# Optimization experiments

Measured on AMD Instinct MI355X. Metric: run time of the kernel, lower is better.

The kernel has to match this reference:

```python
import jax, jax.numpy as jnp
import numpy as np
import math

N_HEADS = 12
D_MODEL = 768
D_HEAD = 64
IGNORE = -100000.0
INIT_STD = 0.02


def setup_inputs() -> dict:
    key = jax.random.key(0)
    ks = jax.random.split(key, 8)
    b, s = 4, 1024
    return {
        "normalized_resid_pre": jax.random.normal(ks[0], (b, 1, s, D_MODEL), jnp.float32),
        "alt_normalized_resid_pre": jax.random.normal(ks[1], (b, s, D_MODEL), jnp.float32),
        "W_Q": jax.random.normal(ks[2], (N_HEADS, D_MODEL, D_HEAD), jnp.float32) * INIT_STD,
        "b_Q": jnp.zeros((N_HEADS, D_HEAD), jnp.float32),
        "W_K": jax.random.normal(ks[3], (N_HEADS, D_MODEL, D_HEAD), jnp.float32) * INIT_STD,
        "b_K": jnp.zeros((N_HEADS, D_HEAD), jnp.float32),
        "W_V": jax.random.normal(ks[4], (N_HEADS, D_MODEL, D_HEAD), jnp.float32) * INIT_STD,
        "b_V": jnp.zeros((N_HEADS, D_HEAD), jnp.float32),
        "W_O": jax.random.normal(ks[5], (N_HEADS, D_HEAD, D_MODEL), jnp.float32) * INIT_STD,
        "b_O": jnp.zeros((D_MODEL,), jnp.float32),
    }


def _apply_attention(x, W_Q, b_Q, W_K, b_K, W_V, b_V, W_O):
    # x: [batch, n_prev(=2), seq, d_model]
    q = jnp.einsum('bpsd,ndh->bpsnh', x, W_Q) + b_Q
    k = jnp.einsum('bpsd,ndh->bpsnh', x, W_K) + b_K
    v = jnp.einsum('bpsd,ndh->bpsnh', x, W_V) + b_V
    scores = jnp.einsum('bpqnh,bpknh->bpnqk', q, k) / math.sqrt(D_HEAD)
    s = scores.shape[-1]
    causal = jnp.triu(jnp.ones((s, s), bool), k=1)  # True above diagonal
    scores = jnp.where(causal, IGNORE, scores)
    pattern = jax.nn.softmax(scores, axis=-1)
    z = jnp.einsum('bpnqk,bpknh->bpqnh', pattern, v)
    # per-head output, NOT summed over heads: [b, p, q, n, d_model]
    return jnp.einsum('bpqnh,nhd->bpqnd', z, W_O)


def reference(normalized_resid_pre, alt_normalized_resid_pre,
              W_Q, b_Q, W_K, b_K, W_V, b_V, W_O, b_O):
    x = jnp.concatenate(
        [normalized_resid_pre, alt_normalized_resid_pre[:, None]], axis=1)  # [b,2,s,d]
    attn_out = _apply_attention(x, W_Q, b_Q, W_K, b_K, W_V, b_V, W_O)  # [b,2,s,n,d]
    old_ablated = attn_out.sum(axis=-2)  # [b,2,s,d]
    orig = attn_out[:, 1]  # [b,s,n,d]
    alt = attn_out[:, 0]   # [b,s,n,d]
    ablate = jnp.ones((N_HEADS, N_HEADS), attn_out.dtype) - jnp.eye(N_HEADS, dtype=attn_out.dtype)
    new_ablated = jnp.einsum('bqnd,kn->bkqd', orig, ablate) + jnp.transpose(alt, (0, 2, 1, 3))
    return jnp.concatenate([old_ablated, new_ablated], axis=1) + b_O  # [b, 2+n_heads, s, d]
```

## Files before the change

kernel.cpp:

```cpp
#include <hip/hip_runtime.h>
#include <math.h>

#define NH 12
#define DM 768
#define DH 64
#define SS 1024

typedef __attribute__((ext_vector_type(8))) short short8;
typedef __attribute__((ext_vector_type(4))) float floatx4;
typedef __attribute__((ext_vector_type(4))) unsigned short usv4;

__device__ __forceinline__ ushort f2bf(float f) {
    union { float f; unsigned u; } v; v.f = f;
    unsigned r = v.u + 0x7fffu + ((v.u >> 16) & 1u);
    return (ushort)(r >> 16);
}
__device__ __forceinline__ float bf2f(ushort u) {
    union { unsigned u; float f; } v; v.u = ((unsigned)u) << 16;
    return v.f;
}

__device__ __forceinline__ void gld_lds16(const ushort* g, ushort* l) {
    __builtin_amdgcn_global_load_lds(
        (const __attribute__((address_space(1))) unsigned int*)g,
        (__attribute__((address_space(3))) unsigned int*)l, 16, 0, 0);
}


__global__ __launch_bounds__(256) void prep_k(
    const float* __restrict__ x0, const float* __restrict__ x1,
    const float* __restrict__ WQ, const float* __restrict__ WK, const float* __restrict__ WV,
    const float* __restrict__ WO,
    ushort* __restrict__ xb, ushort* __restrict__ WbT, ushort* __restrict__ WObT)
{
    __shared__ float T[64][68];
    const int bid = blockIdx.x;
    const int tid = threadIdx.x;
    if (bid < 3072) {
        const size_t e = ((size_t)bid * 256 + tid) * 8;
        const int m = (int)(e / DM), col = (int)(e % DM);
        const int p = (m >> 10) & 1, b = m >> 11, s = m & 1023;
        const float* src = ((p == 0) ? x0 : x1) + (size_t)b * (SS * DM) + (size_t)s * DM + col;
        float4 v0 = *(const float4*)(src);
        float4 v1 = *(const float4*)(src + 4);
        short8 o;
        o[0] = (short)f2bf(v0.x); o[1] = (short)f2bf(v0.y); o[2] = (short)f2bf(v0.z); o[3] = (short)f2bf(v0.w);
        o[4] = (short)f2bf(v1.x); o[5] = (short)f2bf(v1.y); o[6] = (short)f2bf(v1.z); o[7] = (short)f2bf(v1.w);
        *(short8*)(xb + e) = o;
        return;
    }
    const int di = tid >> 2, cg = tid & 3;
    if (bid < 3072 + 432) {
        const int idx = bid - 3072;
        const int tn = idx % 36, dt = idx / 36;
        const int t = tn / NH, n = tn % NH;
        const float* W = ((t == 0) ? WQ : (t == 1) ? WK : WV) + (size_t)n * (DM * DH);
        const int d0 = dt * 64;
#pragma unroll
        for (int j = 0; j < 4; j++) {
            const int c = cg * 16 + j * 4;
            float4 v = *(const float4*)(W + (size_t)(d0 + di) * DH + c);
            *(float4*)&T[di][c] = v;
        }
        __syncthreads();
        ushort* dst = WbT + (size_t)t * (NH * DH * DM) + (size_t)n * (DH * DM) + (size_t)di * DM + d0;
#pragma unroll
        for (int j = 0; j < 4; j++) {
            const int dc = cg * 16 + j * 4;
            usv4 o;
            o[0] = f2bf(T[dc + 0][di]); o[1] = f2bf(T[dc + 1][di]);
            o[2] = f2bf(T[dc + 2][di]); o[3] = f2bf(T[dc + 3][di]);
            *(usv4*)(dst + dc) = o;
        }
        return;
    }
    {
        const int idx = bid - 3072 - 432;
        const int kt = idx % 12, dt = idx / 12;
#pragma unroll
        for (int j = 0; j < 4; j++) {
            const int c = cg * 16 + j * 4;
            float4 v = *(const float4*)(WO + (size_t)(kt * 64 + di) * DM + dt * 64 + c);
            *(float4*)&T[di][c] = v;
        }
        __syncthreads();
        ushort* dst = WObT + (size_t)(dt * 64 + di) * DM + kt * 64;
#pragma unroll
        for (int j = 0; j < 4; j++) {
            const int dc = cg * 16 + j * 4;
            usv4 o;
            o[0] = f2bf(T[dc + 0][di]); o[1] = f2bf(T[dc + 1][di]);
            o[2] = f2bf(T[dc + 2][di]); o[3] = f2bf(T[dc + 3][di]);
            *(usv4*)(dst + dc) = o;
        }
    }
}

__global__ __launch_bounds__(256) void qkv_mfma_k(
    const ushort* __restrict__ xb, const ushort* __restrict__ WbT,
    const float* __restrict__ bQ, const float* __restrict__ bK, const float* __restrict__ bV,
    ushort* __restrict__ Qb, ushort* __restrict__ Kb, ushort* __restrict__ Vtb)
{
    __shared__ ushort As[128 * 32];
    __shared__ ushort Bs[128 * 32];
    const int tid = threadIdx.x;
    const int w = tid >> 6, lane = tid & 63;
    const int l16 = lane & 15, quad = lane >> 4;
    const int jt = blockIdx.x;
    const int mt = blockIdx.y;
    const int t = jt / 6;
    const int jb = (jt % 6) * 128;
    const int mbase = mt * 128;

    const ushort* Bt = WbT + (size_t)t * (DM * DM) + (size_t)jb * DM;

    const int srow = (lane >> 2);
    const int scol = (lane & 3) * 8;
    const ushort* gA0 = xb + (size_t)(mbase + w * 32 + srow) * DM + scol;
    const ushort* gB0 = Bt + (size_t)(w * 32 + srow) * DM + scol;
    ushort* lA0 = As + (w * 32) * 32;
    ushort* lB0 = Bs + (w * 32) * 32;

    floatx4 acc[2][8];
#pragma unroll
    for (int m = 0; m < 2; m++)
#pragma unroll
        for (int n = 0; n < 8; n++) acc[m][n] = (floatx4){0.f, 0.f, 0.f, 0.f};

    for (int kt = 0; kt < 24; kt++) {
        const int k0 = kt * 32;
        __syncthreads();
        gld_lds16(gA0 + k0, lA0);
        gld_lds16(gA0 + (size_t)16 * DM + k0, lA0 + 16 * 32);
        gld_lds16(gB0 + k0, lB0);
        gld_lds16(gB0 + (size_t)16 * DM + k0, lB0 + 16 * 32);
        asm volatile("s_waitcnt vmcnt(0)" ::: "memory");
        __syncthreads();

        const ushort* Ab = As + (w * 32 + l16) * 32 + quad * 8;
        short8 a0 = *(const short8*)(Ab);
        short8 a1 = *(const short8*)(Ab + 16 * 32);
#pragma unroll
        for (int n = 0; n < 8; n++) {
            short8 b = *(const short8*)(Bs + (n * 16 + l16) * 32 + quad * 8);
            acc[0][n] = __builtin_amdgcn_mfma_f32_16x16x32_bf16(a0, b, acc[0][n], 0, 0, 0);
            acc[1][n] = __builtin_amdgcn_mfma_f32_16x16x32_bf16(a1, b, acc[1][n], 0, 0, 0);
        }
    }

    const float* bias = (t == 0) ? bQ : (t == 1) ? bK : bV;
#pragma unroll
    for (int m = 0; m < 2; m++) {
        const int mrow0 = mbase + w * 32 + m * 16 + quad * 4;
        const int bp = mrow0 >> 10;
        const int s0 = mrow0 & 1023;
#pragma unroll
        for (int n = 0; n < 8; n++) {
            const int col = jb + n * 16 + l16;
            const int head = col >> 6, h = col & 63;
            const size_t hb = ((size_t)bp * NH + head) * (SS * DH);
            const float bv = bias[head * DH + h];
            if (t == 0) {
#pragma unroll
                for (int r = 0; r < 4; r++)
                    Qb[hb + (size_t)(s0 + r) * DH + h] = f2bf((acc[m][n][r] + bv) * 0.125f);
            } else if (t == 1) {
#pragma unroll
                for (int r = 0; r < 4; r++)
                    Kb[hb + (size_t)(s0 + r) * DH + h] = f2bf(acc[m][n][r] + bv);
            } else {
                usv4 o;
#pragma unroll
                for (int r = 0; r < 4; r++) o[r] = f2bf(acc[m][n][r] + bv);
                *(usv4*)(Vtb + hb + (size_t)h * SS + s0) = o;
            }
        }
    }
}

__global__ __launch_bounds__(256) void attn_mfma_k(
    const ushort* __restrict__ Qb, const ushort* __restrict__ Kb,
    const ushort* __restrict__ Vtb, ushort* __restrict__ Zb)
{
    __shared__ __align__(16) ushort P_lds[4][16][72];
    const int head = blockIdx.x;
    const int wave = threadIdx.x >> 6;
    const int lane = threadIdx.x & 63;
    const int quad = lane >> 4;
    const int l16  = lane & 15;
    const int qbase = blockIdx.y * 64 + wave * 16;

    const size_t hb = (size_t)head * (SS * DH);
    const ushort* Qh = Qb + hb;
    const ushort* Kh = Kb + hb;
    const ushort* Vh = Vtb + hb;

    short8 a_q0 = *(const short8*)(Qh + (size_t)(qbase + l16) * DH + quad * 8);
    short8 a_q1 = *(const short8*)(Qh + (size_t)(qbase + l16) * DH + 32 + quad * 8);

    floatx4 o[4];
    float m_run[4], l_run[4];
#pragma unroll
    for (int r = 0; r < 4; r++) {
        o[r] = (floatx4){0.f, 0.f, 0.f, 0.f};
        m_run[r] = -1e30f; l_run[r] = 0.f;
    }

    const int kb_last = (qbase + 15) >> 6;
    for (int kb = 0; kb <= kb_last; kb++) {
        floatx4 c[4];
#pragma unroll
        for (int kg = 0; kg < 4; kg++) {
            const ushort* krow = Kh + (size_t)(kb * 64 + kg * 16 + l16) * DH + quad * 8;
            short8 b0 = *(const short8*)(krow);
            short8 b1 = *(const short8*)(krow + 32);
            floatx4 cc = (floatx4){0.f, 0.f, 0.f, 0.f};
            cc = __builtin_amdgcn_mfma_f32_16x16x32_bf16(a_q0, b0, cc, 0, 0, 0);
            cc = __builtin_amdgcn_mfma_f32_16x16x32_bf16(a_q1, b1, cc, 0, 0, 0);
            c[kg] = cc;
        }
        if (kb == kb_last) {
#pragma unroll
            for (int kg = 0; kg < 4; kg++) {
                const int key = kb * 64 + kg * 16 + l16;
#pragma unroll
                for (int r = 0; r < 4; r++) {
                    const int q = qbase + quad * 4 + r;
                    if (key > q) c[kg][r] = -1e30f;
                }
            }
        }
        float mt_[4];
#pragma unroll
        for (int r = 0; r < 4; r++) {
            float m0 = fmaxf(fmaxf(c[0][r], c[1][r]), fmaxf(c[2][r], c[3][r]));
            m0 = fmaxf(m0, __shfl_xor(m0, 1, 64));
            m0 = fmaxf(m0, __shfl_xor(m0, 2, 64));
            m0 = fmaxf(m0, __shfl_xor(m0, 4, 64));
            m0 = fmaxf(m0, __shfl_xor(m0, 8, 64));
            mt_[r] = m0;
        }
        float alpha[4], rs[4];
#pragma unroll
        for (int r = 0; r < 4; r++) {
            const float m_new = fmaxf(m_run[r], mt_[r]);
            alpha[r] = __expf(m_run[r] - m_new);
            m_run[r] = m_new;
            rs[r] = 0.f;
        }
#pragma unroll
        for (int kg = 0; kg < 4; kg++) {
#pragma unroll
            for (int r = 0; r < 4; r++) {
                const float p = __expf(c[kg][r] - m_run[r]);
                rs[r] += p;
                P_lds[wave][quad * 4 + r][kg * 16 + l16] = f2bf(p);
            }
        }
#pragma unroll
        for (int r = 0; r < 4; r++) {
            float s = rs[r];
            s += __shfl_xor(s, 1, 64);
            s += __shfl_xor(s, 2, 64);
            s += __shfl_xor(s, 4, 64);
            s += __shfl_xor(s, 8, 64);
            l_run[r] = l_run[r] * alpha[r] + s;
        }
#pragma unroll
        for (int hg = 0; hg < 4; hg++) {
#pragma unroll
            for (int r = 0; r < 4; r++) o[hg][r] *= alpha[r];
        }
        asm volatile("s_waitcnt lgkmcnt(0)" ::: "memory");
        short8 ap0 = *(const short8*)&P_lds[wave][l16][quad * 8];
        short8 ap1 = *(const short8*)&P_lds[wave][l16][32 + quad * 8];
#pragma unroll
        for (int hg = 0; hg < 4; hg++) {
            const ushort* vrow = Vh + (size_t)(hg * 16 + l16) * SS + kb * 64 + quad * 8;
            short8 bv0 = *(const short8*)(vrow);
            short8 bv1 = *(const short8*)(vrow + 32);
            o[hg] = __builtin_amdgcn_mfma_f32_16x16x32_bf16(ap0, bv0, o[hg], 0, 0, 0);
            o[hg] = __builtin_amdgcn_mfma_f32_16x16x32_bf16(ap1, bv1, o[hg], 0, 0, 0);
        }
        asm volatile("s_waitcnt lgkmcnt(0)" ::: "memory");
    }

    float inv[4];
#pragma unroll
    for (int r = 0; r < 4; r++) inv[r] = 1.f / l_run[r];
#pragma unroll
    for (int hg = 0; hg < 4; hg++) {
#pragma unroll
        for (int r = 0; r < 4; r++) {
            Zb[hb + (size_t)(qbase + quad * 4 + r) * DH + hg * 16 + l16] = f2bf(o[hg][r] * inv[r]);
        }
    }
}

__global__ __launch_bounds__(256) void zdiff_k(
    const ushort* __restrict__ Zb, ushort* __restrict__ Zd)
{
    const size_t e = ((size_t)blockIdx.x * 256 + threadIdx.x) * 8;
    const int bk = (int)(e >> 16);
    const int off = (int)(e & 65535);
    const int b_ = bk / NH, k = bk % NH;
    const ushort* z0 = Zb + ((size_t)(b_ * 2) * NH + k) * (SS * DH) + off;
    const ushort* z1 = Zb + ((size_t)(b_ * 2 + 1) * NH + k) * (SS * DH) + off;
    short8 a = *(const short8*)z0;
    short8 c = *(const short8*)z1;
    short8 o;
#pragma unroll
    for (int i = 0; i < 8; i++)
        o[i] = (short)f2bf(bf2f((ushort)a[i]) - bf2f((ushort)c[i]));
    *(short8*)(Zd + e) = o;
}

__global__ __launch_bounds__(256) void outproj_k(
    const ushort* __restrict__ Zb, const ushort* __restrict__ Zd,
    const ushort* __restrict__ WObT, const float* __restrict__ bO,
    float* __restrict__ out)
{
    __shared__ ushort As[64 * 32];
    __shared__ ushort Bs[128 * 32];
    const int tid = threadIdx.x;
    const int w = tid >> 6, lane = tid & 63;
    const int l16 = lane & 15, quad = lane >> 4;
    const int jb = blockIdx.x * 128;
    const int q0 = blockIdx.y * 64;
    const int b_ = blockIdx.z;

    const int srow = lane >> 2;
    const int scol = (lane & 3) * 8;
    const int arow = q0 + w * 16 + srow;
    const ushort* gB = WObT + (size_t)(jb + w * 32 + srow) * DM + scol;
    ushort* lA = As + (w * 16) * 32;
    ushort* lB0 = Bs + (w * 32) * 32;
    ushort* lB1 = Bs + (w * 32 + 16) * 32;

    const ushort* Afrag = As + (w * 16 + l16) * 32 + quad * 8;

    float bia[8];
#pragma unroll
    for (int n = 0; n < 8; n++) bia[n] = bO[jb + n * 16 + l16];

    floatx4 s1[8];
#pragma unroll 1
    for (int pp = 0; pp < 2; pp++) {
        const ushort* Zp = Zb + (size_t)(b_ * 2 + pp) * (NH * SS * DH);
        floatx4 acc[8];
#pragma unroll
        for (int n = 0; n < 8; n++) acc[n] = (floatx4){0.f, 0.f, 0.f, 0.f};
        for (int kt = 0; kt < 24; kt++) {
            const int k0 = kt * 32;
            __syncthreads();
            gld_lds16(Zp + (size_t)(k0 >> 6) * (SS * DH) + (size_t)arow * DH + (k0 & 63) + scol, lA);
            gld_lds16(gB + k0, lB0);
            gld_lds16(gB + (size_t)16 * DM + k0, lB1);
            asm volatile("s_waitcnt vmcnt(0)" ::: "memory");
            __syncthreads();
            short8 a = *(const short8*)(Afrag);
#pragma unroll
            for (int n = 0; n < 8; n++) {
                short8 b = *(const short8*)(Bs + (n * 16 + l16) * 32 + quad * 8);
                acc[n] = __builtin_amdgcn_mfma_f32_16x16x32_bf16(a, b, acc[n], 0, 0, 0);
            }
        }
        float* obase = out + ((size_t)(b_ * 14 + pp) * SS) * DM;
        const int qr = q0 + w * 16 + quad * 4;
#pragma unroll
        for (int n = 0; n < 8; n++) {
            const int d = jb + n * 16 + l16;
#pragma unroll
            for (int r = 0; r < 4; r++) {
                const float v = acc[n][r] + bia[n];
                obase[(size_t)(qr + r) * DM + d] = v;
                if (pp == 1) s1[n][r] = v;
            }
        }
    }

    const ushort* Zdb = Zd + (size_t)b_ * (NH * SS * DH);
#pragma unroll 1
    for (int k = 0; k < NH; k++) {
        const ushort* Zdk = Zdb + (size_t)k * (SS * DH);
        floatx4 acc[8];
#pragma unroll
        for (int n = 0; n < 8; n++) acc[n] = (floatx4){0.f, 0.f, 0.f, 0.f};
#pragma unroll
        for (int kt = 0; kt < 2; kt++) {
            const int k0 = kt * 32;
            __syncthreads();
            gld_lds16(Zdk + (size_t)arow * DH + k0 + scol, lA);
            gld_lds16(gB + k * DH + k0, lB0);
            gld_lds16(gB + (size_t)16 * DM + k * DH + k0, lB1);
            asm volatile("s_waitcnt vmcnt(0)" ::: "memory");
            __syncthreads();
            short8 a = *(const short8*)(Afrag);
#pragma unroll
            for (int n = 0; n < 8; n++) {
                short8 b = *(const short8*)(Bs + (n * 16 + l16) * 32 + quad * 8);
                acc[n] = __builtin_amdgcn_mfma_f32_16x16x32_bf16(a, b, acc[n], 0, 0, 0);
            }
        }
        float* obase = out + ((size_t)(b_ * 14 + 2 + k) * SS) * DM;
        const int qr = q0 + w * 16 + quad * 4;
#pragma unroll
        for (int n = 0; n < 8; n++) {
            const int d = jb + n * 16 + l16;
#pragma unroll
            for (int r = 0; r < 4; r++)
                obase[(size_t)(qr + r) * DM + d] = acc[n][r] + s1[n][r];
        }
    }
}

extern "C" void kernel_launch(void* const* d_in, const int* in_sizes, int n_in,
                              void* d_out, int out_size, void* d_ws, size_t ws_size,
                              hipStream_t stream)
{
    const float* x0 = (const float*)d_in[0];
    const float* x1 = (const float*)d_in[1];
    const float* WQ = (const float*)d_in[2];
    const float* bQ = (const float*)d_in[3];
    const float* WK = (const float*)d_in[4];
    const float* bK = (const float*)d_in[5];
    const float* WV = (const float*)d_in[6];
    const float* bV = (const float*)d_in[7];
    const float* WO = (const float*)d_in[8];
    const float* bO = (const float*)d_in[9];
    float* out = (float*)d_out;

    ushort* ub   = (ushort*)d_ws;
    ushort* Qb   = ub;
    ushort* Kb   = Qb + 6291456;
    ushort* Vtb  = Kb + 6291456;
    ushort* xb   = Vtb + 6291456;
    ushort* WbT  = xb + 6291456;
    ushort* Zb   = WbT + 1769472;
    ushort* WObT = Zb + 6291456;
    ushort* Zd   = WObT + 589824;

    prep_k<<<dim3(3648), 256, 0, stream>>>(x0, x1, WQ, WK, WV, WO, xb, WbT, WObT);
    qkv_mfma_k<<<dim3(18, 64), 256, 0, stream>>>(xb, WbT, bQ, bK, bV, Qb, Kb, Vtb);
    attn_mfma_k<<<dim3(96, 16), 256, 0, stream>>>(Qb, Kb, Vtb, Zb);
    zdiff_k<<<dim3(1536), 256, 0, stream>>>(Zb, Zd);
    outproj_k<<<dim3(6, 16, 4), 256, 0, stream>>>(Zb, Zd, WObT, bO, out);
}
```

Before: 425.4 us.

## Pair causal query tiles per block and transpose score MFMA for lane-local softmax

Each attention block now handles two query tiles (15-y and y), so every block does the same amount of causal work, and the grid is halved in y. The QK^T MFMA swaps its operands so each lane holds one query row. Row max and row sum then need only two cross-lane shuffles instead of per-register butterfly reductions, and P is written to LDS packed in 32-bit words. V loads are issued before the QK computation to hide their latency. The trade-offs are fewer blocks overall, which may lower occupancy, and extra shuffles to broadcast alpha and the normaliser back to the output layout.

```diff
diff --git a/kernel.cpp b/kernel.cpp
--- a/kernel.cpp
+++ b/kernel.cpp
@@ -188,112 +188,113 @@
     const int lane = threadIdx.x & 63;
     const int quad = lane >> 4;
     const int l16  = lane & 15;
-    const int qbase = blockIdx.y * 64 + wave * 16;
 
     const size_t hb = (size_t)head * (SS * DH);
     const ushort* Qh = Qb + hb;
     const ushort* Kh = Kb + hb;
     const ushort* Vh = Vtb + hb;
 
-    short8 a_q0 = *(const short8*)(Qh + (size_t)(qbase + l16) * DH + quad * 8);
-    short8 a_q1 = *(const short8*)(Qh + (size_t)(qbase + l16) * DH + 32 + quad * 8);
-
-    floatx4 o[4];
-    float m_run[4], l_run[4];
-#pragma unroll
-    for (int r = 0; r < 4; r++) {
-        o[r] = (floatx4){0.f, 0.f, 0.f, 0.f};
-        m_run[r] = -1e30f; l_run[r] = 0.f;
-    }
-
-    const int kb_last = (qbase + 15) >> 6;
-    for (int kb = 0; kb <= kb_last; kb++) {
-        floatx4 c[4];
-#pragma unroll
-        for (int kg = 0; kg < 4; kg++) {
-            const ushort* krow = Kh + (size_t)(kb * 64 + kg * 16 + l16) * DH + quad * 8;
-            short8 b0 = *(const short8*)(krow);
-            short8 b1 = *(const short8*)(krow + 32);
-            floatx4 cc = (floatx4){0.f, 0.f, 0.f, 0.f};
-            cc = __builtin_amdgcn_mfma_f32_16x16x32_bf16(a_q0, b0, cc, 0, 0, 0);
-            cc = __builtin_amdgcn_mfma_f32_16x16x32_bf16(a_q1, b1, cc, 0, 0, 0);
-            c[kg] = cc;
-        }
-        if (kb == kb_last) {
+#pragma unroll 1
+    for (int half = 0; half < 2; half++) {
+        const int qtile = (half == 0) ? (15 - (int)blockIdx.y) : (int)blockIdx.y;
+        const int qbase = qtile * 64 + wave * 16;
+        const int q_lane = qbase + l16;
+
+        short8 b_q0 = *(const short8*)(Qh + (size_t)(qbase + l16) * DH + quad * 8);
+        short8 b_q1 = *(const short8*)(Qh + (size_t)(qbase + l16) * DH + 32 + quad * 8);
+
+        floatx4 o[4];
+        float m_run = -1e30f, l_run = 0.f;
+#pragma unroll
+        for (int hg = 0; hg < 4; hg++) o[hg] = (floatx4){0.f, 0.f, 0.f, 0.f};
+
+        const int kb_last = (qbase + 15) >> 6;
+        for (int kb = 0; kb <= kb_last; kb++) {
+            short8 bv0[4], bv1[4];
+#pragma unroll
+            for (int hg = 0; hg < 4; hg++) {
+                const ushort* vrow = Vh + (size_t)(hg * 16 + l16) * SS + kb * 64 + quad * 8;
+                bv0[hg] = *(const short8*)(vrow);
+                bv1[hg] = *(const short8*)(vrow + 32);
+            }
+
+            floatx4 c[4];
 #pragma unroll
             for (int kg = 0; kg < 4; kg++) {
-                const int key = kb * 64 + kg * 16 + l16;
-#pragma unroll
-                for (int r = 0; r < 4; r++) {
-                    const int q = qbase + quad * 4 + r;
-                    if (key > q) c[kg][r] = -1e30f;
-                }
-            }
-        }
-        float mt_[4];
-#pragma unroll
-        for (int r = 0; r < 4; r++) {
-            float m0 = fmaxf(fmaxf(c[0][r], c[1][r]), fmaxf(c[2][r], c[3][r]));
-            m0 = fmaxf(m0, __shfl_xor(m0, 1, 64));
-            m0 = fmaxf(m0, __shfl_xor(m0, 2, 64));
-            m0 = fmaxf(m0, __shfl_xor(m0, 4, 64));
-            m0 = fmaxf(m0, __shfl_xor(m0, 8, 64));
-            mt_[r] = m0;
-        }
-        float alpha[4], rs[4];
-#pragma unroll
-        for (int r = 0; r < 4; r++) {
-            const float m_new = fmaxf(m_run[r], mt_[r]);
-            alpha[r] = __expf(m_run[r] - m_new);
-            m_run[r] = m_new;
-            rs[r] = 0.f;
-        }
-#pragma unroll
-        for (int kg = 0; kg < 4; kg++) {
-#pragma unroll
-            for (int r = 0; r < 4; r++) {
-                const float p = __expf(c[kg][r] - m_run[r]);
-                rs[r] += p;
-                P_lds[wave][quad * 4 + r][kg * 16 + l16] = f2bf(p);
-            }
-        }
-#pragma unroll
-        for (int r = 0; r < 4; r++) {
-            float s = rs[r];
-            s += __shfl_xor(s, 1, 64);
-            s += __shfl_xor(s, 2, 64);
-            s += __shfl_xor(s, 4, 64);
-            s += __shfl_xor(s, 8, 64);
-            l_run[r] = l_run[r] * alpha[r] + s;
-        }
-#pragma unroll
-        for (int hg = 0; hg < 4; hg++) {
-#pragma unroll
-            for (int r = 0; r < 4; r++) o[hg][r] *= alpha[r];
-        }
-        asm volatile("s_waitcnt lgkmcnt(0)" ::: "memory");
-        short8 ap0 = *(const short8*)&P_lds[wave][l16][quad * 8];
-        short8 ap1 = *(const short8*)&P_lds[wave][l16][32 + quad * 8];
-#pragma unroll
-        for (int hg = 0; hg < 4; hg++) {
-            const ushort* vrow = Vh + (size_t)(hg * 16 + l16) * SS + kb * 64 + quad * 8;
-            short8 bv0 = *(const short8*)(vrow);
-            short8 bv1 = *(const short8*)(vrow + 32);
-            o[hg] = __builtin_amdgcn_mfma_f32_16x16x32_bf16(ap0, bv0, o[hg], 0, 0, 0);
-            o[hg] = __builtin_amdgcn_mfma_f32_16x16x32_bf16(ap1, bv1, o[hg], 0, 0, 0);
-        }
-        asm volatile("s_waitcnt lgkmcnt(0)" ::: "memory");
-    }
-
-    float inv[4];
-#pragma unroll
-    for (int r = 0; r < 4; r++) inv[r] = 1.f / l_run[r];
-#pragma unroll
-    for (int hg = 0; hg < 4; hg++) {
-#pragma unroll
-        for (int r = 0; r < 4; r++) {
-            Zb[hb + (size_t)(qbase + quad * 4 + r) * DH + hg * 16 + l16] = f2bf(o[hg][r] * inv[r]);
-        }
+                const ushort* krow = Kh + (size_t)(kb * 64 + kg * 16 + l16) * DH + quad * 8;
+                short8 k0 = *(const short8*)(krow);
+                short8 k1 = *(const short8*)(krow + 32);
+                floatx4 cc = (floatx4){0.f, 0.f, 0.f, 0.f};
+                cc = __builtin_amdgcn_mfma_f32_16x16x32_bf16(k0, b_q0, cc, 0, 0, 0);
+                cc = __builtin_amdgcn_mfma_f32_16x16x32_bf16(k1, b_q1, cc, 0, 0, 0);
+                c[kg] = cc;
+            }
+            if (kb == kb_last) {
+#pragma unroll
+                for (int kg = 0; kg < 4; kg++)
+#pragma unroll
+                    for (int r = 0; r < 4; r++) {
+                        const int key = kb * 64 + kg * 16 + quad * 4 + r;
+                        if (key > q_lane) c[kg][r] = -1e30f;
+                    }
+            }
+
+            float mk0 = fmaxf(fmaxf(c[0][0], c[0][1]), fmaxf(c[0][2], c[0][3]));
+            float mk1 = fmaxf(fmaxf(c[1][0], c[1][1]), fmaxf(c[1][2], c[1][3]));
+            float mk2 = fmaxf(fmaxf(c[2][0], c[2][1]), fmaxf(c[2][2], c[2][3]));
+            float mk3 = fmaxf(fmaxf(c[3][0], c[3][1]), fmaxf(c[3][2], c[3][3]));
+            float mt = fmaxf(fmaxf(mk0, mk1), fmaxf(mk2, mk3));
+            mt = fmaxf(mt, __shfl_xor(mt, 16, 64));
+            mt = fmaxf(mt, __shfl_xor(mt, 32, 64));
+            const float m_new = fmaxf(m_run, mt);
+            const float alpha = __expf(m_run - m_new);
+            m_run = m_new;
+
+            float rs = 0.f;
+#pragma unroll
+            for (int kg = 0; kg < 4; kg++) {
+                const float p0 = __expf(c[kg][0] - m_new);
+                const float p1 = __expf(c[kg][1] - m_new);
+                const float p2 = __expf(c[kg][2] - m_new);
+                const float p3 = __expf(c[kg][3] - m_new);
+                rs += (p0 + p1) + (p2 + p3);
+                const unsigned w0 = ((unsigned)f2bf(p1) << 16) | (unsigned)f2bf(p0);
+                const unsigned w1 = ((unsigned)f2bf(p3) << 16) | (unsigned)f2bf(p2);
+                *(unsigned*)&P_lds[wave][l16][kg * 16 + quad * 4]     = w0;
+                *(unsigned*)&P_lds[wave][l16][kg * 16 + quad * 4 + 2] = w1;
+            }
+            rs += __shfl_xor(rs, 16, 64);
+            rs += __shfl_xor(rs, 32, 64);
+            l_run = l_run * alpha + rs;
+
+            float a_o[4];
+#pragma unroll
+            for (int r = 0; r < 4; r++) a_o[r] = __shfl(alpha, quad * 4 + r, 64);
+#pragma unroll
+            for (int hg = 0; hg < 4; hg++)
+#pragma unroll
+                for (int r = 0; r < 4; r++) o[hg][r] *= a_o[r];
+
+            asm volatile("s_waitcnt lgkmcnt(0)" ::: "memory");
+            short8 ap0 = *(const short8*)&P_lds[wave][l16][quad * 8];
+            short8 ap1 = *(const short8*)&P_lds[wave][l16][32 + quad * 8];
+#pragma unroll
+            for (int hg = 0; hg < 4; hg++) {
+                o[hg] = __builtin_amdgcn_mfma_f32_16x16x32_bf16(ap0, bv0[hg], o[hg], 0, 0, 0);
+                o[hg] = __builtin_amdgcn_mfma_f32_16x16x32_bf16(ap1, bv1[hg], o[hg], 0, 0, 0);
+            }
+            asm volatile("s_waitcnt lgkmcnt(0)" ::: "memory");
+        }
+
+        const float inv = 1.f / l_run;
+        float inv_o[4];
+#pragma unroll
+        for (int r = 0; r < 4; r++) inv_o[r] = __shfl(inv, quad * 4 + r, 64);
+#pragma unroll
+        for (int hg = 0; hg < 4; hg++)
+#pragma unroll
+            for (int r = 0; r < 4; r++)
+                Zb[hb + (size_t)(qbase + quad * 4 + r) * DH + hg * 16 + l16] = f2bf(o[hg][r] * inv_o[r]);
     }
 }
 
@@ -442,7 +443,7 @@
 
     prep_k<<<dim3(3648), 256, 0, stream>>>(x0, x1, WQ, WK, WV, WO, xb, WbT, WObT);
     qkv_mfma_k<<<dim3(18, 64), 256, 0, stream>>>(xb, WbT, bQ, bK, bV, Qb, Kb, Vtb);
-    attn_mfma_k<<<dim3(96, 16), 256, 0, stream>>>(Qb, Kb, Vtb, Zb);
+    attn_mfma_k<<<dim3(96, 8), 256, 0, stream>>>(Qb, Kb, Vtb, Zb);
     zdiff_k<<<dim3(1536), 256, 0, stream>>>(Zb, Zd);
     outproj_k<<<dim3(6, 16, 4), 256, 0, stream>>>(Zb, Zd, WObT, bO, out);
 }
```

New measurement: 411.9 us. 1.03x faster.
